# Optimization experiments

Hardware: AMD Instinct MI355X
Metric: run time of the kernel (lower is better)

## Reference

```python
import math
import jax, jax.numpy as jnp
import numpy as np

EPS = 1e-6
M, B, K, D, DZ = 4, 2048, 32, 256, 128

def setup_inputs() -> dict:
    key = jax.random.key(0)
    ks = jax.random.split(key, 8)
    return {
        "h_nei": jax.random.normal(ks[0], (M, B, K, D), jnp.float32),
        "ew_anc": jax.random.uniform(ks[1], (B, K, M), jnp.float32),
        "view_mask": jnp.ones((B, K, M), jnp.float32),
        "z_anc": jax.random.normal(ks[2], (B, DZ), jnp.float32),
        "lbl_delta": jax.random.normal(ks[3], (B, K, M, D), jnp.float32),
        "lbl_weight": jax.random.normal(ks[4], (B, K, M), jnp.float32) * 0.1,
        "W_Q": jax.random.normal(ks[5], (DZ, D), jnp.float32) / math.sqrt(DZ),
        "W_K": jax.random.normal(ks[6], (M, D, D), jnp.float32) / math.sqrt(D),
        "W_V": jax.random.normal(ks[7], (M, D, D), jnp.float32) / math.sqrt(D),
        "log_vw": jnp.zeros((M,), jnp.float32),
    }

def reference(h_nei, ew_anc, view_mask, z_anc, lbl_delta, lbl_weight, W_Q, W_K, W_V, log_vw):
    # Cross-attention mode (use_query_z=True). Dropout is identity (eval mode).
    d = h_nei.shape[-1]
    Q = z_anc @ W_Q                                            # [B, d]
    Kx = jnp.einsum('mbkd,mde->mbke', h_nei, W_K)              # [M, B, K, d]
    Vx = jnp.einsum('mbkd,mde->mbke', h_nei, W_V)
    Vx = Vx + jnp.moveaxis(lbl_delta, 2, 0)                    # add lbl_delta[:,:,m,:]
    ew = jnp.moveaxis(ew_anc, 2, 0)                            # [M, B, K]
    lw = jnp.moveaxis(lbl_weight, 2, 0)
    vm = jnp.moveaxis(view_mask, 2, 0)
    scores = jnp.einsum('bd,mbkd->mbk', Q, Kx) / math.sqrt(d)
    scores = scores + jnp.log(ew + EPS) + lw
    scores = jnp.where(vm == 0, -1e9, scores)
    attn = jax.nn.softmax(scores, axis=-1)                     # [M, B, K]
    ctx_m = jnp.einsum('mbk,mbkd->mbd', attn, Vx)              # [M, B, d]
    vw = jax.nn.softmax(log_vw)                                # [M]
    return jnp.einsum('m,mbd->bd', vw, ctx_m)                  # [B, d]
```

## Files before the change

### kernel.cpp

```cpp
#include <hip/hip_runtime.h>
#include <hip/hip_bf16.h>
#include <math.h>

#define M_  4
#define B_  2048
#define K_  32
#define D_  256
#define DZ_ 128
#define PAD 68

__global__ void __launch_bounds__(256) k0_wqk(const float* __restrict__ W_Q,
                                              const float* __restrict__ W_K,
                                              float* __restrict__ Wqk) {
    int mz = blockIdx.x;
    int m = mz >> 7, z = mz & 127;
    int d = threadIdx.x;
    __shared__ float wq[D_];
    wq[d] = W_Q[z * D_ + d];
    __syncthreads();
    const float* wk = W_K + (m * D_ + d) * D_;
    float acc = 0.f;
#pragma unroll 8
    for (int e = 0; e < D_; ++e) acc = fmaf(wq[e], wk[e], acc);
    Wqk[(m * DZ_ + z) * D_ + d] = acc;
}

__global__ void __launch_bounds__(256) k1_qk(const float* __restrict__ z_anc,
                                             const float* __restrict__ Wqk,
                                             float* __restrict__ Qk) {
    int m = blockIdx.z;
    int b0 = blockIdx.x * 64, d0 = blockIdx.y * 64;
    int t = threadIdx.x, tx = t & 15, ty = t >> 4;
    __shared__ float As[64 * PAD];
    __shared__ float Bs[64 * PAD];
    float c[4][4] = {};
    for (int kc = 0; kc < DZ_; kc += 64) {
#pragma unroll
        for (int it = 0; it < 4; ++it) {
            int s = it * 256 + t, bi = s >> 4, k4 = (s & 15) * 4;
            *(float4*)&As[bi * PAD + k4] =
                *(const float4*)&z_anc[(b0 + bi) * DZ_ + kc + k4];
        }
#pragma unroll
        for (int it = 0; it < 4; ++it) {
            int s = it * 256 + t, kk = s >> 4, d4 = (s & 15) * 4;
            *(float4*)&Bs[kk * PAD + d4] =
                *(const float4*)&Wqk[(m * DZ_ + kc + kk) * D_ + d0 + d4];
        }
        __syncthreads();
#pragma unroll 4
        for (int kk = 0; kk < 64; ++kk) {
            float a[4];
#pragma unroll
            for (int i = 0; i < 4; ++i) a[i] = As[(ty * 4 + i) * PAD + kk];
            float4 b4 = *(const float4*)&Bs[kk * PAD + tx * 4];
#pragma unroll
            for (int i = 0; i < 4; ++i) {
                c[i][0] = fmaf(a[i], b4.x, c[i][0]);
                c[i][1] = fmaf(a[i], b4.y, c[i][1]);
                c[i][2] = fmaf(a[i], b4.z, c[i][2]);
                c[i][3] = fmaf(a[i], b4.w, c[i][3]);
            }
        }
        __syncthreads();
    }
#pragma unroll
    for (int i = 0; i < 4; ++i) {
        float4 v = make_float4(c[i][0], c[i][1], c[i][2], c[i][3]);
        *(float4*)&Qk[(m * B_ + b0 + ty * 4 + i) * D_ + d0 + tx * 4] = v;
    }
}

__device__ __forceinline__ void gl_lds16(const float* g, float* lds) {
    __builtin_amdgcn_global_load_lds(
        (const __attribute__((address_space(1))) void*)g,
        (__attribute__((address_space(3))) void*)lds, 16, 0, 0);
}

__global__ void __launch_bounds__(256) k2_main(
    const float* __restrict__ h_nei, const float* __restrict__ ew_anc,
    const float* __restrict__ vmask, const float* __restrict__ lbl_delta,
    const float* __restrict__ lbl_w, const float* __restrict__ Qk,
    const float* __restrict__ log_vw,
    float* __restrict__ hbar, float* __restrict__ lblp)
{
    int bm = blockIdx.x;
    int b = bm >> 2, m = bm & 3;
    int t = threadIdx.x, w = t >> 6, l = t & 63;
    __shared__ float hs[K_ * D_];
    __shared__ float ls[K_ * D_];
    __shared__ float sc[K_], at[K_];

    const float* hb  = h_nei + ((size_t)(m * B_ + b)) * (K_ * D_);
    const float* ldb = lbl_delta + (size_t)b * (K_ * M_ * D_) + m * D_;
#pragma unroll
    for (int j = 0; j < 8; ++j) {
        int k = w * 8 + j;
        gl_lds16(hb + k * D_ + 4 * l, hs + k * D_);
        gl_lds16(ldb + (size_t)k * (M_ * D_) + 4 * l, ls + k * D_);
    }

    float4 q4 = *(const float4*)&Qk[(m * B_ + b) * D_ + 4 * l];
    float ew_v = 0.f, lw_v = 0.f, vm_v = 1.f;
    if (t < K_) {
        int idx = (b * K_ + t) * M_ + m;
        ew_v = ew_anc[idx];
        lw_v = lbl_w[idx];
        vm_v = vmask[idx];
    }
    float lv0 = log_vw[0], lv1 = log_vw[1], lv2 = log_vw[2], lv3 = log_vw[3];
    float mv = fmaxf(fmaxf(lv0, lv1), fmaxf(lv2, lv3));
    float e0 = expf(lv0 - mv), e1 = expf(lv1 - mv),
          e2 = expf(lv2 - mv), e3 = expf(lv3 - mv);
    float vw_m = ((m == 0) ? e0 : (m == 1) ? e1 : (m == 2) ? e2 : e3)
                 / (e0 + e1 + e2 + e3);

    __syncthreads();

#pragma unroll
    for (int j = 0; j < 8; ++j) {
        int k = w * 8 + j;
        float4 h4 = *(const float4*)&hs[k * D_ + 4 * l];
        float v = h4.x * q4.x + h4.y * q4.y + h4.z * q4.z + h4.w * q4.w;
        v += __shfl_xor(v, 32); v += __shfl_xor(v, 16); v += __shfl_xor(v, 8);
        v += __shfl_xor(v, 4);  v += __shfl_xor(v, 2);  v += __shfl_xor(v, 1);
        if (l == 0) sc[k] = v;
    }
    __syncthreads();

    if (t < K_) {
        float s = (vm_v == 0.f) ? -1e9f
                                : sc[t] * 0.0625f + logf(ew_v + 1e-6f) + lw_v;
        float mx = s;
        mx = fmaxf(mx, __shfl_xor(mx, 16)); mx = fmaxf(mx, __shfl_xor(mx, 8));
        mx = fmaxf(mx, __shfl_xor(mx, 4));  mx = fmaxf(mx, __shfl_xor(mx, 2));
        mx = fmaxf(mx, __shfl_xor(mx, 1));
        float ee = expf(s - mx);
        float ds = ee;
        ds += __shfl_xor(ds, 16); ds += __shfl_xor(ds, 8); ds += __shfl_xor(ds, 4);
        ds += __shfl_xor(ds, 2);  ds += __shfl_xor(ds, 1);
        at[t] = (ee / ds) * vw_m;
    }
    __syncthreads();

    float ah = 0.f, al = 0.f;
#pragma unroll 8
    for (int k = 0; k < K_; ++k) {
        float a = at[k];
        ah = fmaf(a, hs[k * D_ + t], ah);
        al = fmaf(a, ls[k * D_ + t], al);
    }
    hbar[(size_t)b * (M_ * D_) + m * D_ + t] = ah;
    lblp[((size_t)m * B_ + b) * D_ + t] = al;
}

__global__ void __launch_bounds__(256) k3_gemm(const float* __restrict__ hbar,
                                               const float* __restrict__ W_V,
                                               const float* __restrict__ lblp,
                                               float* __restrict__ out) {
    int b0 = blockIdx.x * 16, e0 = blockIdx.y * 64;
    int t = threadIdx.x, tx = t & 15, ty = t >> 4;
    __shared__ float As[16 * PAD];
    __shared__ float Bs[64 * PAD];
    float c0 = 0.f, c1 = 0.f, c2 = 0.f, c3 = 0.f;
    for (int kc = 0; kc < M_ * D_; kc += 64) {
        {
            int bi = t >> 4, k4 = (t & 15) * 4;
            *(float4*)&As[bi * PAD + k4] =
                *(const float4*)&hbar[(size_t)(b0 + bi) * (M_ * D_) + kc + k4];
        }
#pragma unroll
        for (int it = 0; it < 4; ++it) {
            int s = it * 256 + t, kk = s >> 4, e4 = (s & 15) * 4;
            *(float4*)&Bs[kk * PAD + e4] =
                *(const float4*)&W_V[(size_t)(kc + kk) * D_ + e0 + e4];
        }
        __syncthreads();
#pragma unroll 4
        for (int kk = 0; kk < 64; ++kk) {
            float a0 = As[ty * PAD + kk];
            float4 b4 = *(const float4*)&Bs[kk * PAD + tx * 4];
            c0 = fmaf(a0, b4.x, c0);
            c1 = fmaf(a0, b4.y, c1);
            c2 = fmaf(a0, b4.z, c2);
            c3 = fmaf(a0, b4.w, c3);
        }
        __syncthreads();
    }
    int row = b0 + ty, col = e0 + tx * 4;
    float4 s = make_float4(c0, c1, c2, c3);
#pragma unroll
    for (int mm = 0; mm < 4; ++mm) {
        float4 lp = *(const float4*)&lblp[((size_t)mm * B_ + row) * D_ + col];
        s.x += lp.x; s.y += lp.y; s.z += lp.z; s.w += lp.w;
    }
    *(float4*)&out[(size_t)row * D_ + col] = s;
}

extern "C" void kernel_launch(void* const* d_in, const int* in_sizes, int n_in,
                              void* d_out, int out_size, void* d_ws, size_t ws_size,
                              hipStream_t stream) {
    const float* h_nei     = (const float*)d_in[0];
    const float* ew_anc    = (const float*)d_in[1];
    const float* vmask     = (const float*)d_in[2];
    const float* z_anc     = (const float*)d_in[3];
    const float* lbl_delta = (const float*)d_in[4];
    const float* lbl_w     = (const float*)d_in[5];
    const float* W_Q       = (const float*)d_in[6];
    const float* W_K       = (const float*)d_in[7];
    const float* W_V       = (const float*)d_in[8];
    const float* log_vw    = (const float*)d_in[9];
    float* out = (float*)d_out;

    float* ws   = (float*)d_ws;
    float* Wqk  = ws;
    float* Qk   = Wqk + (M_ * DZ_ * D_);
    float* hbar = Qk + (M_ * B_ * D_);
    float* lblp = hbar + (B_ * M_ * D_);

    k0_wqk<<<M_ * DZ_, 256, 0, stream>>>(W_Q, W_K, Wqk);

    dim3 g1(B_ / 64, D_ / 64, M_);
    k1_qk<<<g1, 256, 0, stream>>>(z_anc, Wqk, Qk);

    k2_main<<<B_ * M_, 256, 0, stream>>>(h_nei, ew_anc, vmask, lbl_delta,
                                         lbl_w, Qk, log_vw, hbar, lblp);

    dim3 g3(B_ / 16, D_ / 64);
    k3_gemm<<<g3, 256, 0, stream>>>(hbar, W_V, lblp, out);
}
```

Before: 179.1 us.

## Make attention kernel persistent with double-buffered LDS prefetch across pairs

The per-(b,m) attention kernel becomes a persistent kernel: 256 blocks of 512 threads each process 32 consecutive (b,m) pairs. While the current pair is computed, the next pair's h_nei and lbl_delta tiles are prefetched into a second LDS buffer using global_load_lds, gated by manual vmcnt waits and barriers. Attention weights are broadcast with readlane, and the h and lbl reductions are split across the two halves of the block. The aim is to overlap memory streaming with compute and avoid per-block launch and ramp-up costs. In exchange, only one block fits per CU because of the large LDS footprint, so fewer loads may be in flight, and the hand-written waitcnt ordering is fragile.

```diff
diff --git a/kernel.cpp b/kernel.cpp
--- a/kernel.cpp
+++ b/kernel.cpp
@@ -8,6 +8,9 @@
 #define D_  256
 #define DZ_ 128
 #define PAD 68
+
+#define K2_SMEM_FLOATS (4 * 8192 + 32)
+#define K2_SMEM_BYTES  (K2_SMEM_FLOATS * 4)
 
 __global__ void __launch_bounds__(256) k0_wqk(const float* __restrict__ W_Q,
                                               const float* __restrict__ W_K,
@@ -77,81 +80,115 @@
         (__attribute__((address_space(3))) void*)lds, 16, 0, 0);
 }
 
-__global__ void __launch_bounds__(256) k2_main(
+__global__ void __launch_bounds__(512, 1) k2_main(
     const float* __restrict__ h_nei, const float* __restrict__ ew_anc,
     const float* __restrict__ vmask, const float* __restrict__ lbl_delta,
     const float* __restrict__ lbl_w, const float* __restrict__ Qk,
     const float* __restrict__ log_vw,
     float* __restrict__ hbar, float* __restrict__ lblp)
 {
-    int bm = blockIdx.x;
-    int b = bm >> 2, m = bm & 3;
+    extern __shared__ float smem[];
+    float* sc = smem + 32768;
+
     int t = threadIdx.x, w = t >> 6, l = t & 63;
-    __shared__ float hs[K_ * D_];
-    __shared__ float ls[K_ * D_];
-    __shared__ float sc[K_], at[K_];
-
-    const float* hb  = h_nei + ((size_t)(m * B_ + b)) * (K_ * D_);
-    const float* ldb = lbl_delta + (size_t)b * (K_ * M_ * D_) + m * D_;
-#pragma unroll
-    for (int j = 0; j < 8; ++j) {
-        int k = w * 8 + j;
-        gl_lds16(hb + k * D_ + 4 * l, hs + k * D_);
-        gl_lds16(ldb + (size_t)k * (M_ * D_) + 4 * l, ls + k * D_);
-    }
-
-    float4 q4 = *(const float4*)&Qk[(m * B_ + b) * D_ + 4 * l];
-    float ew_v = 0.f, lw_v = 0.f, vm_v = 1.f;
-    if (t < K_) {
-        int idx = (b * K_ + t) * M_ + m;
-        ew_v = ew_anc[idx];
-        lw_v = lbl_w[idx];
-        vm_v = vmask[idx];
-    }
+    int base = blockIdx.x * 32;
+
     float lv0 = log_vw[0], lv1 = log_vw[1], lv2 = log_vw[2], lv3 = log_vw[3];
     float mv = fmaxf(fmaxf(lv0, lv1), fmaxf(lv2, lv3));
     float e0 = expf(lv0 - mv), e1 = expf(lv1 - mv),
           e2 = expf(lv2 - mv), e3 = expf(lv3 - mv);
-    float vw_m = ((m == 0) ? e0 : (m == 1) ? e1 : (m == 2) ? e2 : e3)
-                 / (e0 + e1 + e2 + e3);
-
-    __syncthreads();
-
-#pragma unroll
-    for (int j = 0; j < 8; ++j) {
-        int k = w * 8 + j;
-        float4 h4 = *(const float4*)&hs[k * D_ + 4 * l];
-        float v = h4.x * q4.x + h4.y * q4.y + h4.z * q4.z + h4.w * q4.w;
-        v += __shfl_xor(v, 32); v += __shfl_xor(v, 16); v += __shfl_xor(v, 8);
-        v += __shfl_xor(v, 4);  v += __shfl_xor(v, 2);  v += __shfl_xor(v, 1);
-        if (l == 0) sc[k] = v;
-    }
-    __syncthreads();
-
-    if (t < K_) {
-        float s = (vm_v == 0.f) ? -1e9f
-                                : sc[t] * 0.0625f + logf(ew_v + 1e-6f) + lw_v;
+    float den = e0 + e1 + e2 + e3;
+    float vw0 = e0 / den, vw1 = e1 / den, vw2 = e2 / den, vw3 = e3 / den;
+
+    float4 q4c; float ewc, lwc, vmc;
+    {
+        int g = base; int b = g >> 2, m = g & 3;
+        q4c = *(const float4*)&Qk[(m * B_ + b) * D_ + 4 * l];
+        int idx = (b * K_ + (l & 31)) * M_ + m;
+        ewc = ew_anc[idx]; lwc = lbl_w[idx]; vmc = vmask[idx];
+        const float* hb  = h_nei + (size_t)(m * B_ + b) * (K_ * D_);
+        const float* ldb = lbl_delta + (size_t)b * (K_ * M_ * D_) + m * D_;
+#pragma unroll
+        for (int j = 0; j < 4; ++j) {
+            int k = w * 4 + j;
+            gl_lds16(hb + k * D_ + 4 * l, smem + k * D_);
+            gl_lds16(ldb + (size_t)k * (M_ * D_) + 4 * l, smem + 16384 + k * D_);
+        }
+    }
+
+    for (int it = 0; it < 32; ++it) {
+        int curo = (it & 1) ? 8192 : 0;
+        int nxto = curo ^ 8192;
+        int nxt = (it + 1) & 31;
+
+        float4 q4n; float ewn, lwn, vmn;
+        {
+            int g = base + nxt; int b = g >> 2, m = g & 3;
+            q4n = *(const float4*)&Qk[(m * B_ + b) * D_ + 4 * l];
+            int idx = (b * K_ + (l & 31)) * M_ + m;
+            ewn = ew_anc[idx]; lwn = lbl_w[idx]; vmn = vmask[idx];
+            const float* hb  = h_nei + (size_t)(m * B_ + b) * (K_ * D_);
+            const float* ldb = lbl_delta + (size_t)b * (K_ * M_ * D_) + m * D_;
+#pragma unroll
+            for (int j = 0; j < 4; ++j) {
+                int k = w * 4 + j;
+                gl_lds16(hb + k * D_ + 4 * l, smem + nxto + k * D_);
+                gl_lds16(ldb + (size_t)k * (M_ * D_) + 4 * l,
+                         smem + 16384 + nxto + k * D_);
+            }
+        }
+
+        asm volatile("s_waitcnt vmcnt(8)" ::: "memory");
+        __builtin_amdgcn_sched_barrier(0);
+        __builtin_amdgcn_s_barrier();
+
+        const float* hd  = smem + curo;
+        const float* ld_ = smem + 16384 + curo;
+
+#pragma unroll
+        for (int j = 0; j < 4; ++j) {
+            int k = w * 4 + j;
+            float4 h4 = *(const float4*)&hd[k * D_ + 4 * l];
+            float v = h4.x * q4c.x + h4.y * q4c.y + h4.z * q4c.z + h4.w * q4c.w;
+            v += __shfl_xor(v, 32); v += __shfl_xor(v, 16); v += __shfl_xor(v, 8);
+            v += __shfl_xor(v, 4);  v += __shfl_xor(v, 2);  v += __shfl_xor(v, 1);
+            if (l == 0) sc[k] = v;
+        }
+        asm volatile("s_waitcnt lgkmcnt(0)" ::: "memory");
+        __builtin_amdgcn_sched_barrier(0);
+        __builtin_amdgcn_s_barrier();
+
+        int g = base + it; int b = g >> 2, m = g & 3;
+        float vw_m = (m == 0) ? vw0 : (m == 1) ? vw1 : (m == 2) ? vw2 : vw3;
+        float s = sc[l & 31] * 0.0625f + logf(ewc + 1e-6f) + lwc;
+        if (vmc == 0.f) s = -1e9f;
         float mx = s;
         mx = fmaxf(mx, __shfl_xor(mx, 16)); mx = fmaxf(mx, __shfl_xor(mx, 8));
         mx = fmaxf(mx, __shfl_xor(mx, 4));  mx = fmaxf(mx, __shfl_xor(mx, 2));
         mx = fmaxf(mx, __shfl_xor(mx, 1));
         float ee = expf(s - mx);
-        float ds = ee;
-        ds += __shfl_xor(ds, 16); ds += __shfl_xor(ds, 8); ds += __shfl_xor(ds, 4);
-        ds += __shfl_xor(ds, 2);  ds += __shfl_xor(ds, 1);
-        at[t] = (ee / ds) * vw_m;
-    }
-    __syncthreads();
-
-    float ah = 0.f, al = 0.f;
-#pragma unroll 8
-    for (int k = 0; k < K_; ++k) {
-        float a = at[k];
-        ah = fmaf(a, hs[k * D_ + t], ah);
-        al = fmaf(a, ls[k * D_ + t], al);
-    }
-    hbar[(size_t)b * (M_ * D_) + m * D_ + t] = ah;
-    lblp[((size_t)m * B_ + b) * D_ + t] = al;
+        float dsum = ee;
+        dsum += __shfl_xor(dsum, 16); dsum += __shfl_xor(dsum, 8);
+        dsum += __shfl_xor(dsum, 4);  dsum += __shfl_xor(dsum, 2);
+        dsum += __shfl_xor(dsum, 1);
+        float atv = (ee / dsum) * vw_m;
+
+        float acc = 0.f;
+        const float* src = (t < 256) ? hd : ld_;
+        int col = t & 255;
+#pragma unroll
+        for (int k = 0; k < K_; ++k) {
+            float a = __int_as_float(
+                __builtin_amdgcn_readlane(__float_as_int(atv), k));
+            acc = fmaf(a, src[k * D_ + col], acc);
+        }
+        if (t < 256) hbar[(size_t)b * (M_ * D_) + m * D_ + col] = acc;
+        else         lblp[((size_t)m * B_ + b) * D_ + col] = acc;
+
+        q4c = q4n; ewc = ewn; lwc = lwn; vmc = vmn;
+
+        __builtin_amdgcn_s_barrier();
+    }
 }
 
 __global__ void __launch_bounds__(256) k3_gemm(const float* __restrict__ hbar,
@@ -218,13 +255,17 @@
     float* hbar = Qk + (M_ * B_ * D_);
     float* lblp = hbar + (B_ * M_ * D_);
 
+    (void)hipFuncSetAttribute((const void*)k2_main,
+                              hipFuncAttributeMaxDynamicSharedMemorySize,
+                              K2_SMEM_BYTES);
+
     k0_wqk<<<M_ * DZ_, 256, 0, stream>>>(W_Q, W_K, Wqk);
 
     dim3 g1(B_ / 64, D_ / 64, M_);
     k1_qk<<<g1, 256, 0, stream>>>(z_anc, Wqk, Qk);
 
-    k2_main<<<B_ * M_, 256, 0, stream>>>(h_nei, ew_anc, vmask, lbl_delta,
-                                         lbl_w, Qk, log_vw, hbar, lblp);
+    k2_main<<<256, 512, K2_SMEM_BYTES, stream>>>(
+        h_nei, ew_anc, vmask, lbl_delta, lbl_w, Qk, log_vw, hbar, lblp);
 
     dim3 g3(B_ / 16, D_ / 64);
     k3_gemm<<<g3, 256, 0, stream>>>(hbar, W_V, lblp, out);
```

Result: slower. 224.5 us (+25.3%).

## Split main kernel into h_nei attention pass and contiguous lbl_delta reduction pass

Applied to the files above, without the earlier changes.

The fused per-(b,m) kernel is split in two. The first computes the attention weights and the h reduction, writing the weights to a workspace. The second reads lbl_delta in contiguous 16-row chunks across all views, where the old kernel did strided per-view reads, and each block holds 64KB of LDS. This buys more coalesced lbl_delta traffic and smaller per-block LDS in the first kernel, at the cost of an extra launch, a workspace round trip, and twice as many partial lblp buffers read in the final GEMM.

```diff
diff --git a/kernel.cpp b/kernel.cpp
--- a/kernel.cpp
+++ b/kernel.cpp
@@ -77,37 +77,27 @@
         (__attribute__((address_space(3))) void*)lds, 16, 0, 0);
 }
 
-__global__ void __launch_bounds__(256) k2_main(
+__global__ void __launch_bounds__(256) k2h(
     const float* __restrict__ h_nei, const float* __restrict__ ew_anc,
-    const float* __restrict__ vmask, const float* __restrict__ lbl_delta,
-    const float* __restrict__ lbl_w, const float* __restrict__ Qk,
-    const float* __restrict__ log_vw,
-    float* __restrict__ hbar, float* __restrict__ lblp)
+    const float* __restrict__ vmask, const float* __restrict__ lbl_w,
+    const float* __restrict__ Qk, const float* __restrict__ log_vw,
+    float* __restrict__ hbar, float* __restrict__ at_ws)
 {
-    int bm = blockIdx.x;
-    int b = bm >> 2, m = bm & 3;
+    int bx = blockIdx.x;
+    int b = bx & (B_ - 1), m = bx >> 11;
     int t = threadIdx.x, w = t >> 6, l = t & 63;
     __shared__ float hs[K_ * D_];
-    __shared__ float ls[K_ * D_];
-    __shared__ float sc[K_], at[K_];
-
-    const float* hb  = h_nei + ((size_t)(m * B_ + b)) * (K_ * D_);
-    const float* ldb = lbl_delta + (size_t)b * (K_ * M_ * D_) + m * D_;
+    __shared__ float sc[K_], at_l[K_];
+
+    const float* hb = h_nei + (size_t)(m * B_ + b) * (K_ * D_);
 #pragma unroll
     for (int j = 0; j < 8; ++j) {
         int k = w * 8 + j;
         gl_lds16(hb + k * D_ + 4 * l, hs + k * D_);
-        gl_lds16(ldb + (size_t)k * (M_ * D_) + 4 * l, ls + k * D_);
-    }
-
+    }
     float4 q4 = *(const float4*)&Qk[(m * B_ + b) * D_ + 4 * l];
-    float ew_v = 0.f, lw_v = 0.f, vm_v = 1.f;
-    if (t < K_) {
-        int idx = (b * K_ + t) * M_ + m;
-        ew_v = ew_anc[idx];
-        lw_v = lbl_w[idx];
-        vm_v = vmask[idx];
-    }
+    int idx = (b * K_ + (l & 31)) * M_ + m;
+    float ew_v = ew_anc[idx], lw_v = lbl_w[idx], vm_v = vmask[idx];
     float lv0 = log_vw[0], lv1 = log_vw[1], lv2 = log_vw[2], lv3 = log_vw[3];
     float mv = fmaxf(fmaxf(lv0, lv1), fmaxf(lv2, lv3));
     float e0 = expf(lv0 - mv), e1 = expf(lv1 - mv),
@@ -128,35 +118,73 @@
     }
     __syncthreads();
 
+    float s = (vm_v == 0.f) ? -1e9f
+                            : sc[l & 31] * 0.0625f + logf(ew_v + 1e-6f) + lw_v;
+    float mx = s;
+    mx = fmaxf(mx, __shfl_xor(mx, 16)); mx = fmaxf(mx, __shfl_xor(mx, 8));
+    mx = fmaxf(mx, __shfl_xor(mx, 4));  mx = fmaxf(mx, __shfl_xor(mx, 2));
+    mx = fmaxf(mx, __shfl_xor(mx, 1));
+    float ee = expf(s - mx);
+    float dsum = ee;
+    dsum += __shfl_xor(dsum, 16); dsum += __shfl_xor(dsum, 8);
+    dsum += __shfl_xor(dsum, 4);  dsum += __shfl_xor(dsum, 2);
+    dsum += __shfl_xor(dsum, 1);
+    float atv = (ee / dsum) * vw_m;
+
     if (t < K_) {
-        float s = (vm_v == 0.f) ? -1e9f
-                                : sc[t] * 0.0625f + logf(ew_v + 1e-6f) + lw_v;
-        float mx = s;
-        mx = fmaxf(mx, __shfl_xor(mx, 16)); mx = fmaxf(mx, __shfl_xor(mx, 8));
-        mx = fmaxf(mx, __shfl_xor(mx, 4));  mx = fmaxf(mx, __shfl_xor(mx, 2));
-        mx = fmaxf(mx, __shfl_xor(mx, 1));
-        float ee = expf(s - mx);
-        float ds = ee;
-        ds += __shfl_xor(ds, 16); ds += __shfl_xor(ds, 8); ds += __shfl_xor(ds, 4);
-        ds += __shfl_xor(ds, 2);  ds += __shfl_xor(ds, 1);
-        at[t] = (ee / ds) * vw_m;
-    }
-    __syncthreads();
-
-    float ah = 0.f, al = 0.f;
+        at_l[t] = atv;
+        at_ws[(size_t)(m * B_ + b) * K_ + t] = atv;
+    }
+    __syncthreads();
+
+    float acc = 0.f;
 #pragma unroll 8
-    for (int k = 0; k < K_; ++k) {
-        float a = at[k];
-        ah = fmaf(a, hs[k * D_ + t], ah);
-        al = fmaf(a, ls[k * D_ + t], al);
-    }
-    hbar[(size_t)b * (M_ * D_) + m * D_ + t] = ah;
-    lblp[((size_t)m * B_ + b) * D_ + t] = al;
+    for (int k = 0; k < K_; ++k) acc = fmaf(at_l[k], hs[k * D_ + t], acc);
+    hbar[(size_t)b * (M_ * D_) + m * D_ + t] = acc;
+}
+
+__global__ void __launch_bounds__(512) k2l(
+    const float* __restrict__ lbl_delta, const float* __restrict__ at_ws,
+    float* __restrict__ lblp2)
+{
+    extern __shared__ float smem2[];
+    float* ls = smem2;
+    float* at_l = smem2 + 16 * M_ * D_;
+
+    int bx = blockIdx.x;
+    int b = bx >> 1, kh = bx & 1;
+    int t = threadIdx.x, w = t >> 6, l = t & 63;
+
+    const float* ldb = lbl_delta + (size_t)b * (K_ * M_ * D_)
+                                 + (size_t)kh * 16 * M_ * D_;
+#pragma unroll
+    for (int j = 0; j < 8; ++j) {
+        int r = w * 8 + j;
+        gl_lds16(ldb + r * D_ + 4 * l, ls + r * D_);
+    }
+    if (t < 64) {
+        int m = t >> 4, kk = t & 15;
+        at_l[t] = at_ws[(size_t)(m * B_ + b) * K_ + kh * 16 + kk];
+    }
+    __syncthreads();
+
+    int m = t >> 7, d = t & 127;
+    float a1 = 0.f, a2 = 0.f;
+#pragma unroll 8
+    for (int kk = 0; kk < 16; ++kk) {
+        float a = at_l[m * 16 + kk];
+        int base = (kk * M_ + m) * D_;
+        a1 = fmaf(a, ls[base + d], a1);
+        a2 = fmaf(a, ls[base + 128 + d], a2);
+    }
+    size_t o = ((size_t)(kh * M_ + m) * B_ + b) * D_;
+    lblp2[o + d] = a1;
+    lblp2[o + 128 + d] = a2;
 }
 
 __global__ void __launch_bounds__(256) k3_gemm(const float* __restrict__ hbar,
                                                const float* __restrict__ W_V,
-                                               const float* __restrict__ lblp,
+                                               const float* __restrict__ lblp2,
                                                float* __restrict__ out) {
     int b0 = blockIdx.x * 16, e0 = blockIdx.y * 64;
     int t = threadIdx.x, tx = t & 15, ty = t >> 4;
@@ -190,8 +218,8 @@
     int row = b0 + ty, col = e0 + tx * 4;
     float4 s = make_float4(c0, c1, c2, c3);
 #pragma unroll
-    for (int mm = 0; mm < 4; ++mm) {
-        float4 lp = *(const float4*)&lblp[((size_t)mm * B_ + row) * D_ + col];
+    for (int q = 0; q < 8; ++q) {
+        float4 lp = *(const float4*)&lblp2[((size_t)q * B_ + row) * D_ + col];
         s.x += lp.x; s.y += lp.y; s.z += lp.z; s.w += lp.w;
     }
     *(float4*)&out[(size_t)row * D_ + col] = s;
@@ -212,20 +240,28 @@
     const float* log_vw    = (const float*)d_in[9];
     float* out = (float*)d_out;
 
-    float* ws   = (float*)d_ws;
-    float* Wqk  = ws;
-    float* Qk   = Wqk + (M_ * DZ_ * D_);
-    float* hbar = Qk + (M_ * B_ * D_);
-    float* lblp = hbar + (B_ * M_ * D_);
+    float* ws    = (float*)d_ws;
+    float* Wqk   = ws;
+    float* Qk    = Wqk + (M_ * DZ_ * D_);
+    float* hbar  = Qk + (M_ * B_ * D_);
+    float* at_ws = hbar + (B_ * M_ * D_);
+    float* lblp2 = at_ws + (M_ * B_ * K_);
+
+    (void)hipFuncSetAttribute((const void*)k2l,
+                              hipFuncAttributeMaxDynamicSharedMemorySize,
+                              (16 * M_ * D_ + 64) * 4);
 
     k0_wqk<<<M_ * DZ_, 256, 0, stream>>>(W_Q, W_K, Wqk);
 
     dim3 g1(B_ / 64, D_ / 64, M_);
     k1_qk<<<g1, 256, 0, stream>>>(z_anc, Wqk, Qk);
 
-    k2_main<<<B_ * M_, 256, 0, stream>>>(h_nei, ew_anc, vmask, lbl_delta,
-                                         lbl_w, Qk, log_vw, hbar, lblp);
+    k2h<<<M_ * B_, 256, 0, stream>>>(h_nei, ew_anc, vmask, lbl_w, Qk, log_vw,
+                                     hbar, at_ws);
+
+    k2l<<<B_ * 2, 512, (16 * M_ * D_ + 64) * 4, stream>>>(lbl_delta, at_ws,
+                                                          lblp2);
 
     dim3 g3(B_ / 16, D_ / 64);
-    k3_gemm<<<g3, 256, 0, stream>>>(hbar, W_V, lblp, out);
-}
+    k3_gemm<<<g3, 256, 0, stream>>>(hbar, W_V, lblp2, out);
+}
```

Measured after the change: 180.4 us. Within noise of the previous version (+0.7%).
